# Kernel optimization log

Measured on AMD Instinct MI355X. Metric: run time of the kernel, lower is better.

The kernel has to match this reference:

```python
import jax, jax.numpy as jnp
import numpy as np

TOKEN_DIM = 256
N_HEADS = 8
HEAD_DIM = TOKEN_DIM // N_HEADS


def setup_inputs() -> dict:
    key = jax.random.key(0)
    ks = jax.random.split(key, 10)
    B, S, D = 4, 2048, TOKEN_DIM
    s = 1.0 / np.sqrt(D)
    return {
        "x": jax.random.normal(ks[0], (B, S, D), dtype=jnp.float32),
        "Wq": jax.random.uniform(ks[1], (D, D), jnp.float32, -s, s),
        "bq": jax.random.uniform(ks[2], (D,), jnp.float32, -s, s),
        "Wk": jax.random.uniform(ks[3], (D, D), jnp.float32, -s, s),
        "bk": jax.random.uniform(ks[4], (D,), jnp.float32, -s, s),
        "Wv": jax.random.uniform(ks[5], (D, D), jnp.float32, -s, s),
        "bv": jax.random.uniform(ks[6], (D,), jnp.float32, -s, s),
        "Wo": jax.random.uniform(ks[7], (D, D), jnp.float32, -s, s),
        "bo": jax.random.uniform(ks[8], (D,), jnp.float32, -s, s),
        "head_scale": jnp.ones((N_HEADS,), dtype=jnp.float32),
    }


def reference(x, Wq, bq, Wk, bk, Wv, bv, Wo, bo, head_scale):
    B, S, D = x.shape
    H, Hd = N_HEADS, HEAD_DIM
    scale = jnp.asarray(np.sqrt(Hd), x.dtype)

    def split_heads(t):
        return t.reshape(B, S, H, Hd).transpose(0, 2, 1, 3)  # (B,H,S,Hd)

    Q = split_heads(x @ Wq.T + bq)
    K = split_heads(x @ Wk.T + bk)
    V = split_heads(x @ Wv.T + bv)

    scores = jnp.einsum("bhsd,bhtd->bhst", Q, K) / scale  # (B,H,S,S)
    attn = jax.nn.softmax(scores, axis=-1)
    attn_scaled = attn * head_scale[None, :, None, None]
    Hctx = jnp.einsum("bhst,bhtd->bhsd", attn_scaled, V)
    Hctx = Hctx.transpose(0, 2, 1, 3).reshape(B, S, D)
    return Hctx @ Wo.T + bo
```

## Files before the change

### kernel.cpp

```cpp
#include <hip/hip_runtime.h>
#include <hip/hip_bf16.h>
#include <math.h>

#define B_ 4
#define S_ 2048
#define D_ 256
#define H_ 8
#define HD_ 32

typedef __attribute__((ext_vector_type(8))) short short8;
typedef __attribute__((ext_vector_type(4))) short short4v;
typedef __attribute__((ext_vector_type(4))) float floatx4;
typedef unsigned short ushort_t;
typedef unsigned int uint_t;

typedef union { unsigned u[2]; short4v v4; } PkU;

#define CVT_PK(DST, LO, HI) \
  asm volatile("v_cvt_pk_bf16_f32 %0, %1, %2" : "=v"(DST) : "v"(LO), "v"(HI))

#define MFMA16(ACC, A, B) \
  asm volatile("v_mfma_f32_16x16x16_bf16 %0, %1, %2, %0" : "+v"(ACC) : "v"(A), "v"(B))

__device__ __forceinline__ ushort_t f2bf(float f) {
  union { float f; unsigned u; } v; v.f = f;
  unsigned u = v.u;
  unsigned r = (u + 0x7FFFu + ((u >> 16) & 1u)) >> 16;
  return (ushort_t)r;
}

__global__ __launch_bounds__(256)
void cvt_all(const float* __restrict__ x,
             const float* __restrict__ wq, const float* __restrict__ wk,
             const float* __restrict__ wv, const float* __restrict__ wo,
             ushort_t* __restrict__ xb,
             ushort_t* __restrict__ wqb, ushort_t* __restrict__ wkb,
             ushort_t* __restrict__ wvb, ushort_t* __restrict__ wob)
{
  const int b = blockIdx.x;
  const float4* s; uint2* d; int i;
  if (b < 2048) {
    s = (const float4*)x; d = (uint2*)xb; i = b * 256 + threadIdx.x;
  } else {
    int r = b - 2048; int mm = r >> 6;
    s = (const float4*)(mm == 0 ? wq : mm == 1 ? wk : mm == 2 ? wv : wo);
    d = (uint2*)(mm == 0 ? wqb : mm == 1 ? wkb : mm == 2 ? wvb : wob);
    i = (r & 63) * 256 + threadIdx.x;
  }
  float4 f = s[i];
  uint2 o;
  CVT_PK(o.x, f.x, f.y);
  CVT_PK(o.y, f.z, f.w);
  d[i] = o;
}

__global__ __launch_bounds__(256)
void proj_qkv(const ushort_t* __restrict__ xb,
              const ushort_t* __restrict__ wq, const ushort_t* __restrict__ wk, const ushort_t* __restrict__ wv,
              const float* __restrict__ bq, const float* __restrict__ bk, const float* __restrict__ bv,
              ushort_t* __restrict__ qout, ushort_t* __restrict__ kout, ushort_t* __restrict__ vout)
{
  __shared__ __align__(16) ushort_t W_lds[64 * 264];

  const int z = blockIdx.z;
  const ushort_t* wb = (z == 0) ? wq : (z == 1) ? wk : wv;
  const float* bias  = (z == 0) ? bq : (z == 1) ? bk : bv;

  const int t = threadIdx.x;
  const int l = t & 63;
  const int w = t >> 6;
  const int row0 = blockIdx.y * 128 + w * 16;
  const int col0 = blockIdx.x * 64;
  const int lr = l & 15, lg = l >> 4, lk = lg * 8;

  {
    const ushort_t* wsrc = wb + (col0 + (t >> 2)) * D_ + (t & 3) * 64;
    ushort_t* wdst = &W_lds[(t >> 2) * 264 + (t & 3) * 64];
#pragma unroll
    for (int i = 0; i < 8; ++i)
      *(uint4*)(wdst + i * 8) = *(const uint4*)(wsrc + i * 8);
  }
  __syncthreads();

  floatx4 acc[2][4] = {};
  const ushort_t* arow0 = xb + (row0 + lr) * D_ + lk;
  const ushort_t* arow1 = xb + (row0 + 64 + lr) * D_ + lk;
#pragma unroll
  for (int kk = 0; kk < D_; kk += 32) {
    short8 a0 = *(const short8*)(arow0 + kk);
    short8 a1 = *(const short8*)(arow1 + kk);
#pragma unroll
    for (int j = 0; j < 4; ++j) {
      short8 b = *(const short8*)&W_lds[(j * 16 + lr) * 264 + kk + lk];
      acc[0][j] = __builtin_amdgcn_mfma_f32_16x16x32_bf16(a0, b, acc[0][j], 0, 0, 0);
      acc[1][j] = __builtin_amdgcn_mfma_f32_16x16x32_bf16(a1, b, acc[1][j], 0, 0, 0);
    }
  }

  if (z == 2) {
#pragma unroll
    for (int rs = 0; rs < 2; ++rs)
#pragma unroll
      for (int j = 0; j < 4; ++j) {
        int c = col0 + j * 16 + lr;
        float bv_ = bias[c];
        int hh = c >> 5, d = c & 31;
        int i0 = row0 + rs * 64 + lg * 4;
        int bb = i0 >> 11, s0 = i0 & 2047;
        uint2 pv;
        CVT_PK(pv.x, acc[rs][j][0] + bv_, acc[rs][j][1] + bv_);
        CVT_PK(pv.y, acc[rs][j][2] + bv_, acc[rs][j][3] + bv_);
        *(uint2*)&vout[(((size_t)(bb * H_ + hh)) * HD_ + d) * S_ + s0] = pv;
      }
  } else {
    ushort_t* dst = (z == 0) ? qout : kout;
    const float qscale = (z == 0) ? 0.25503486f : 1.0f;
#pragma unroll
    for (int rs = 0; rs < 2; ++rs)
#pragma unroll
      for (int j = 0; j < 4; ++j) {
        int c = col0 + j * 16 + lr;
        float bv_ = bias[c];
        int hh = c >> 5, d = c & 31;
#pragma unroll
        for (int rp = 0; rp < 2; ++rp) {
          int i = row0 + rs * 64 + lg * 4 + rp * 2;
          int bb = i >> 11, s = i & 2047;
          uint_t pr;
          CVT_PK(pr, (acc[rs][j][rp*2] + bv_) * qscale, (acc[rs][j][rp*2+1] + bv_) * qscale);
          size_t b0 = ((size_t)(bb * H_ + hh) * S_ + s) * HD_ + d;
          dst[b0]       = (ushort_t)(pr & 0xffffu);
          dst[b0 + HD_] = (ushort_t)(pr >> 16);
        }
      }
  }
}

__global__ __launch_bounds__(256)
void attn_kernel(const ushort_t* __restrict__ qb, const ushort_t* __restrict__ kb,
                 const ushort_t* __restrict__ vtb, const float* __restrict__ head_scale,
                 ushort_t* __restrict__ hb)
{
  __shared__ __align__(16) ushort_t K_lds[2][128 * 40];
  __shared__ __align__(16) ushort_t Vt_lds[2][32 * 140];

  const int tid = threadIdx.x;
  const int l = tid & 63;
  const int w = tid >> 6;
  const int f = blockIdx.y * 32 + blockIdx.x;
  const int qt = f >> 5;
  const int bh = (f & 7) * 4 + ((f >> 3) & 3);
  const int lr = l & 15;
  const int lg = l >> 4;

  const ushort_t* qp  = qb  + (size_t)bh * S_ * HD_;
  const ushort_t* kp  = kb  + (size_t)bh * S_ * HD_;
  const ushort_t* vtp = vtb + (size_t)bh * S_ * HD_;

  const int q0 = qt * 64 + w * 16;
  short8 qfrag = *(const short8*)(qp + (q0 + lr) * HD_ + lg * 8);

  floatx4 oA = {}, oB = {}, oL = {};

  const int kr = tid >> 1, kc = (tid & 1) * 16;
  const int vr = tid >> 3, vc = (tid & 7) * 16;

  const short4v ones4 = {0x3F80, 0x3F80, 0x3F80, 0x3F80};
  const floatx4 zero4 = {0.f, 0.f, 0.f, 0.f};

  uint4 kr0 = *(const uint4*)(kp + kr * HD_ + kc);
  uint4 kr1 = *(const uint4*)(kp + kr * HD_ + kc + 8);
  uint4 vv0 = *(const uint4*)(vtp + vr * S_ + vc);
  uint4 vv1 = *(const uint4*)(vtp + vr * S_ + vc + 8);
  *(uint4*)&K_lds[0][kr * 40 + kc]     = kr0;
  *(uint4*)&K_lds[0][kr * 40 + kc + 8] = kr1;
  {
    ushort_t* vd = &Vt_lds[0][vr * 140 + vc];
    *(uint2*)(vd)      = make_uint2(vv0.x, vv0.y);
    *(uint2*)(vd + 4)  = make_uint2(vv0.z, vv0.w);
    *(uint2*)(vd + 8)  = make_uint2(vv1.x, vv1.y);
    *(uint2*)(vd + 12) = make_uint2(vv1.z, vv1.w);
  }

  int cur = 0;
  for (int t0 = 0; t0 < S_; t0 += 128) {
    __syncthreads();

    const int tn = (t0 + 128) & (S_ - 1);
    kr0 = *(const uint4*)(kp + (tn + kr) * HD_ + kc);
    kr1 = *(const uint4*)(kp + (tn + kr) * HD_ + kc + 8);
    vv0 = *(const uint4*)(vtp + vr * S_ + tn + vc);
    vv1 = *(const uint4*)(vtp + vr * S_ + tn + vc + 8);

    floatx4 sv[8];
#pragma unroll
    for (int s = 0; s < 8; ++s) {
      short8 kf = *(const short8*)&K_lds[cur][(s * 16 + lr) * 40 + lg * 8];
      sv[s] = __builtin_amdgcn_mfma_f32_16x16x32_bf16(kf, qfrag, zero4, 0, 0, 0);
    }

    PkU pk[8];
    __builtin_amdgcn_s_setprio(1);
#pragma unroll
    for (int s = 0; s < 2; ++s) {
      sv[s][0] = __builtin_amdgcn_exp2f(sv[s][0]);
      sv[s][1] = __builtin_amdgcn_exp2f(sv[s][1]);
      sv[s][2] = __builtin_amdgcn_exp2f(sv[s][2]);
      sv[s][3] = __builtin_amdgcn_exp2f(sv[s][3]);
    }
    CVT_PK(pk[0].u[0], sv[0][0], sv[0][1]);
    CVT_PK(pk[0].u[1], sv[0][2], sv[0][3]);
    CVT_PK(pk[1].u[0], sv[1][0], sv[1][1]);
    CVT_PK(pk[1].u[1], sv[1][2], sv[1][3]);
#pragma unroll
    for (int s = 0; s < 8; ++s) {
      const int cb = s * 16 + lg * 4;
      short4v a0 = *(const short4v*)&Vt_lds[cur][lr * 140 + cb];
      short4v a1 = *(const short4v*)&Vt_lds[cur][(16 + lr) * 140 + cb];
      MFMA16(oA, a0, pk[s].v4);
      MFMA16(oB, a1, pk[s].v4);
      MFMA16(oL, ones4, pk[s].v4);
      if (s + 2 < 8) {
        sv[s+2][0] = __builtin_amdgcn_exp2f(sv[s+2][0]);
        sv[s+2][1] = __builtin_amdgcn_exp2f(sv[s+2][1]);
        sv[s+2][2] = __builtin_amdgcn_exp2f(sv[s+2][2]);
        sv[s+2][3] = __builtin_amdgcn_exp2f(sv[s+2][3]);
        CVT_PK(pk[s+2].u[0], sv[s+2][0], sv[s+2][1]);
        CVT_PK(pk[s+2].u[1], sv[s+2][2], sv[s+2][3]);
      }
    }
    __builtin_amdgcn_s_setprio(0);

    *(uint4*)&K_lds[cur ^ 1][kr * 40 + kc]     = kr0;
    *(uint4*)&K_lds[cur ^ 1][kr * 40 + kc + 8] = kr1;
    {
      ushort_t* vd = &Vt_lds[cur ^ 1][vr * 140 + vc];
      *(uint2*)(vd)      = make_uint2(vv0.x, vv0.y);
      *(uint2*)(vd + 4)  = make_uint2(vv0.z, vv0.w);
      *(uint2*)(vd + 8)  = make_uint2(vv1.x, vv1.y);
      *(uint2*)(vd + 12) = make_uint2(vv1.z, vv1.w);
    }
    cur ^= 1;
  }

  asm volatile("s_nop 7\n\ts_nop 7" :::);
  const int bb = bh >> 3, hh = bh & 7;
  float inv = head_scale[hh] / oL[0];
  const int sq = q0 + lr;
  size_t base = ((size_t)(bb * S_ + sq)) * D_ + hh * HD_;
  uint2 w0, w1;
  CVT_PK(w0.x, oA[0] * inv, oA[1] * inv);
  CVT_PK(w0.y, oA[2] * inv, oA[3] * inv);
  CVT_PK(w1.x, oB[0] * inv, oB[1] * inv);
  CVT_PK(w1.y, oB[2] * inv, oB[3] * inv);
  *(uint2*)&hb[base + lg * 4] = w0;
  *(uint2*)&hb[base + 16 + lg * 4] = w1;
}

__global__ __launch_bounds__(256)
void proj_out(const ushort_t* __restrict__ hbm, const ushort_t* __restrict__ wo,
              const float* __restrict__ bo, float* __restrict__ out)
{
  __shared__ __align__(16) ushort_t W_lds[64 * 264];

  const int t = threadIdx.x;
  const int l = t & 63;
  const int w = t >> 6;
  const int row0 = blockIdx.y * 64 + w * 16;
  const int col0 = blockIdx.x * 64;
  const int lr = l & 15, lg = l >> 4, lk = lg * 8;

  {
    const ushort_t* wsrc = wo + (col0 + (t >> 2)) * D_ + (t & 3) * 64;
    ushort_t* wdst = &W_lds[(t >> 2) * 264 + (t & 3) * 64];
#pragma unroll
    for (int i = 0; i < 8; ++i)
      *(uint4*)(wdst + i * 8) = *(const uint4*)(wsrc + i * 8);
  }
  __syncthreads();

  floatx4 acc[4] = {};
  const ushort_t* arow = hbm + (row0 + lr) * D_ + lk;
#pragma unroll
  for (int kk = 0; kk < D_; kk += 32) {
    short8 a = *(const short8*)(arow + kk);
#pragma unroll
    for (int j = 0; j < 4; ++j) {
      short8 b = *(const short8*)&W_lds[(j * 16 + lr) * 264 + kk + lk];
      acc[j] = __builtin_amdgcn_mfma_f32_16x16x32_bf16(a, b, acc[j], 0, 0, 0);
    }
  }
#pragma unroll
  for (int j = 0; j < 4; ++j) {
    int c = col0 + j * 16 + lr;
    float bias = bo[c];
#pragma unroll
    for (int r = 0; r < 4; ++r) {
      int i = row0 + lg * 4 + r;
      out[(size_t)i * D_ + c] = acc[j][r] + bias;
    }
  }
}

extern "C" void kernel_launch(void* const* d_in, const int* in_sizes, int n_in,
                              void* d_out, int out_size, void* d_ws, size_t ws_size,
                              hipStream_t stream) {
  (void)in_sizes; (void)n_in; (void)out_size; (void)ws_size;
  const float* x  = (const float*)d_in[0];
  const float* Wq = (const float*)d_in[1];
  const float* bq = (const float*)d_in[2];
  const float* Wk = (const float*)d_in[3];
  const float* bk = (const float*)d_in[4];
  const float* Wv = (const float*)d_in[5];
  const float* bv = (const float*)d_in[6];
  const float* Wo = (const float*)d_in[7];
  const float* bo = (const float*)d_in[8];
  const float* hs = (const float*)d_in[9];

  char* ws = (char*)d_ws;
  ushort_t* xb  = (ushort_t*)ws;
  ushort_t* wqb = (ushort_t*)(ws + 4 * 1024 * 1024);
  ushort_t* wkb = wqb + 65536;
  ushort_t* wvb = wkb + 65536;
  ushort_t* wob = wvb + 65536;
  ushort_t* qb  = wob + 65536;
  ushort_t* kbb = qb + 2097152;
  ushort_t* vbb = kbb + 2097152;
  ushort_t* hbb = xb;

  cvt_all<<<2304, 256, 0, stream>>>(x, Wq, Wk, Wv, Wo, xb, wqb, wkb, wvb, wob);
  proj_qkv<<<dim3(4, 64, 3), 256, 0, stream>>>(xb, wqb, wkb, wvb, bq, bk, bv, qb, kbb, vbb);
  attn_kernel<<<dim3(32, 32), 256, 0, stream>>>(qb, kbb, vbb, hs, hbb);
  proj_out<<<dim3(4, 128), 256, 0, stream>>>(hbb, wob, bo, (float*)d_out);
}
```

Baseline: 62.18 us.

## Process two query groups per attention block and double proj_out row tile

The attention kernel now computes two 64-query groups per block against each staged K/V tile, halving the grid and the number of times K/V are loaded into LDS per query. The output projection likewise computes 128 rows per block, reusing each Wo LDS fragment for two MFMAs. The cost is more accumulator registers per thread and half as many blocks, which lowers the number of waves available to hide latency on the GPU.

```diff
diff --git a/kernel.cpp b/kernel.cpp
--- a/kernel.cpp
+++ b/kernel.cpp
@@ -147,7 +147,7 @@
   const int tid = threadIdx.x;
   const int l = tid & 63;
   const int w = tid >> 6;
-  const int f = blockIdx.y * 32 + blockIdx.x;
+  const int f = blockIdx.y * 16 + blockIdx.x;
   const int qt = f >> 5;
   const int bh = (f & 7) * 4 + ((f >> 3) & 3);
   const int lr = l & 15;
@@ -157,10 +157,13 @@
   const ushort_t* kp  = kb  + (size_t)bh * S_ * HD_;
   const ushort_t* vtp = vtb + (size_t)bh * S_ * HD_;
 
-  const int q0 = qt * 64 + w * 16;
-  short8 qfrag = *(const short8*)(qp + (q0 + lr) * HD_ + lg * 8);
-
-  floatx4 oA = {}, oB = {}, oL = {};
+  const int qA = qt * 128 + w * 16;
+  const int qB = qA + 64;
+  short8 qfragA = *(const short8*)(qp + (qA + lr) * HD_ + lg * 8);
+  short8 qfragB = *(const short8*)(qp + (qB + lr) * HD_ + lg * 8);
+
+  floatx4 oAA = {}, oBA = {}, oLA = {};
+  floatx4 oAB = {}, oBB = {}, oLB = {};
 
   const int kr = tid >> 1, kc = (tid & 1) * 16;
   const int vr = tid >> 3, vc = (tid & 7) * 16;
@@ -183,24 +186,15 @@
   }
 
   int cur = 0;
-  for (int t0 = 0; t0 < S_; t0 += 128) {
-    __syncthreads();
-
-    const int tn = (t0 + 128) & (S_ - 1);
-    kr0 = *(const uint4*)(kp + (tn + kr) * HD_ + kc);
-    kr1 = *(const uint4*)(kp + (tn + kr) * HD_ + kc + 8);
-    vv0 = *(const uint4*)(vtp + vr * S_ + tn + vc);
-    vv1 = *(const uint4*)(vtp + vr * S_ + tn + vc + 8);
-
+
+  auto run_group = [&](short8 qf, floatx4& oA, floatx4& oB, floatx4& oL) {
     floatx4 sv[8];
 #pragma unroll
     for (int s = 0; s < 8; ++s) {
       short8 kf = *(const short8*)&K_lds[cur][(s * 16 + lr) * 40 + lg * 8];
-      sv[s] = __builtin_amdgcn_mfma_f32_16x16x32_bf16(kf, qfrag, zero4, 0, 0, 0);
-    }
-
+      sv[s] = __builtin_amdgcn_mfma_f32_16x16x32_bf16(kf, qf, zero4, 0, 0, 0);
+    }
     PkU pk[8];
-    __builtin_amdgcn_s_setprio(1);
 #pragma unroll
     for (int s = 0; s < 2; ++s) {
       sv[s][0] = __builtin_amdgcn_exp2f(sv[s][0]);
@@ -229,6 +223,20 @@
         CVT_PK(pk[s+2].u[1], sv[s+2][2], sv[s+2][3]);
       }
     }
+  };
+
+  for (int t0 = 0; t0 < S_; t0 += 128) {
+    __syncthreads();
+
+    const int tn = (t0 + 128) & (S_ - 1);
+    kr0 = *(const uint4*)(kp + (tn + kr) * HD_ + kc);
+    kr1 = *(const uint4*)(kp + (tn + kr) * HD_ + kc + 8);
+    vv0 = *(const uint4*)(vtp + vr * S_ + tn + vc);
+    vv1 = *(const uint4*)(vtp + vr * S_ + tn + vc + 8);
+
+    __builtin_amdgcn_s_setprio(1);
+    run_group(qfragA, oAA, oBA, oLA);
+    run_group(qfragB, oAB, oBB, oLB);
     __builtin_amdgcn_s_setprio(0);
 
     *(uint4*)&K_lds[cur ^ 1][kr * 40 + kc]     = kr0;
@@ -245,16 +253,29 @@
 
   asm volatile("s_nop 7\n\ts_nop 7" :::);
   const int bb = bh >> 3, hh = bh & 7;
-  float inv = head_scale[hh] / oL[0];
-  const int sq = q0 + lr;
-  size_t base = ((size_t)(bb * S_ + sq)) * D_ + hh * HD_;
-  uint2 w0, w1;
-  CVT_PK(w0.x, oA[0] * inv, oA[1] * inv);
-  CVT_PK(w0.y, oA[2] * inv, oA[3] * inv);
-  CVT_PK(w1.x, oB[0] * inv, oB[1] * inv);
-  CVT_PK(w1.y, oB[2] * inv, oB[3] * inv);
-  *(uint2*)&hb[base + lg * 4] = w0;
-  *(uint2*)&hb[base + 16 + lg * 4] = w1;
+  const float hsc = head_scale[hh];
+  {
+    float inv = hsc / oLA[0];
+    size_t base = ((size_t)(bb * S_ + qA + lr)) * D_ + hh * HD_;
+    uint2 w0, w1;
+    CVT_PK(w0.x, oAA[0] * inv, oAA[1] * inv);
+    CVT_PK(w0.y, oAA[2] * inv, oAA[3] * inv);
+    CVT_PK(w1.x, oBA[0] * inv, oBA[1] * inv);
+    CVT_PK(w1.y, oBA[2] * inv, oBA[3] * inv);
+    *(uint2*)&hb[base + lg * 4] = w0;
+    *(uint2*)&hb[base + 16 + lg * 4] = w1;
+  }
+  {
+    float inv = hsc / oLB[0];
+    size_t base = ((size_t)(bb * S_ + qB + lr)) * D_ + hh * HD_;
+    uint2 w0, w1;
+    CVT_PK(w0.x, oAB[0] * inv, oAB[1] * inv);
+    CVT_PK(w0.y, oAB[2] * inv, oAB[3] * inv);
+    CVT_PK(w1.x, oBB[0] * inv, oBB[1] * inv);
+    CVT_PK(w1.y, oBB[2] * inv, oBB[3] * inv);
+    *(uint2*)&hb[base + lg * 4] = w0;
+    *(uint2*)&hb[base + 16 + lg * 4] = w1;
+  }
 }
 
 __global__ __launch_bounds__(256)
@@ -266,7 +287,7 @@
   const int t = threadIdx.x;
   const int l = t & 63;
   const int w = t >> 6;
-  const int row0 = blockIdx.y * 64 + w * 16;
+  const int row0 = blockIdx.y * 128 + w * 16;
   const int col0 = blockIdx.x * 64;
   const int lr = l & 15, lg = l >> 4, lk = lg * 8;
 
@@ -279,27 +300,32 @@
   }
   __syncthreads();
 
-  floatx4 acc[4] = {};
-  const ushort_t* arow = hbm + (row0 + lr) * D_ + lk;
+  floatx4 acc[2][4] = {};
+  const ushort_t* arow0 = hbm + (row0 + lr) * D_ + lk;
+  const ushort_t* arow1 = hbm + (row0 + 64 + lr) * D_ + lk;
 #pragma unroll
   for (int kk = 0; kk < D_; kk += 32) {
-    short8 a = *(const short8*)(arow + kk);
+    short8 a0 = *(const short8*)(arow0 + kk);
+    short8 a1 = *(const short8*)(arow1 + kk);
 #pragma unroll
     for (int j = 0; j < 4; ++j) {
       short8 b = *(const short8*)&W_lds[(j * 16 + lr) * 264 + kk + lk];
-      acc[j] = __builtin_amdgcn_mfma_f32_16x16x32_bf16(a, b, acc[j], 0, 0, 0);
-    }
-  }
-#pragma unroll
-  for (int j = 0; j < 4; ++j) {
-    int c = col0 + j * 16 + lr;
-    float bias = bo[c];
-#pragma unroll
-    for (int r = 0; r < 4; ++r) {
-      int i = row0 + lg * 4 + r;
-      out[(size_t)i * D_ + c] = acc[j][r] + bias;
-    }
-  }
+      acc[0][j] = __builtin_amdgcn_mfma_f32_16x16x32_bf16(a0, b, acc[0][j], 0, 0, 0);
+      acc[1][j] = __builtin_amdgcn_mfma_f32_16x16x32_bf16(a1, b, acc[1][j], 0, 0, 0);
+    }
+  }
+#pragma unroll
+  for (int rs = 0; rs < 2; ++rs)
+#pragma unroll
+    for (int j = 0; j < 4; ++j) {
+      int c = col0 + j * 16 + lr;
+      float bias = bo[c];
+#pragma unroll
+      for (int r = 0; r < 4; ++r) {
+        int i = row0 + rs * 64 + lg * 4 + r;
+        out[(size_t)i * D_ + c] = acc[rs][j][r] + bias;
+      }
+    }
 }
 
 extern "C" void kernel_launch(void* const* d_in, const int* in_sizes, int n_in,
@@ -330,6 +356,6 @@
 
   cvt_all<<<2304, 256, 0, stream>>>(x, Wq, Wk, Wv, Wo, xb, wqb, wkb, wvb, wob);
   proj_qkv<<<dim3(4, 64, 3), 256, 0, stream>>>(xb, wqb, wkb, wvb, bq, bk, bv, qb, kbb, vbb);
-  attn_kernel<<<dim3(32, 32), 256, 0, stream>>>(qb, kbb, vbb, hs, hbb);
-  proj_out<<<dim3(4, 128), 256, 0, stream>>>(hbb, wob, bo, (float*)d_out);
-}
+  attn_kernel<<<dim3(16, 32), 256, 0, stream>>>(qb, kbb, vbb, hs, hbb);
+  proj_out<<<dim3(4, 64), 256, 0, stream>>>(hbb, wob, bo, (float*)d_out);
+}
```

After: 65.28 us. 1.05x slower.
